# Performance work log

Measured on AMD Instinct MI355X. Metric: run time of the kernel, lower is better.

The kernel has to match this reference:

```python
import jax, jax.numpy as jnp
import numpy as np

SCALE = 256.0  # emulates SharedFxpShift = 8 fixed-point shift


def requant(x):
    # RequantFxpToScaledInt8: shift down by SharedFxpShift and clamp to int8 range
    return jnp.clip(x / SCALE, -128.0, 127.0)


def prelu(x, a):
    return jnp.where(x >= 0, x, a * x)


def _linearize(c):
    # injective encoding of 3D int coords (coords in [-8, 2040) after +8 shift)
    c = c.astype(jnp.int64) + 8
    B = 2048
    return (c[:, 0] * B + c[:, 1]) * B + c[:, 2]


def sparse_conv(coords, feats, W, stride):
    # 3x3x3 submanifold sparse conv: for each kernel offset, hash-lookup the
    # neighbor via sorted linearized coords + searchsorted, gather, matmul.
    # coords [N,3] int32, feats [N,Cin], W [27,Cin,Cout]
    lin = _linearize(coords)
    perm = jnp.argsort(lin)
    slin = lin[perm]
    N = coords.shape[0]
    out = jnp.zeros((N, W.shape[-1]), feats.dtype)
    k = 0
    for dx in (-1, 0, 1):
        for dy in (-1, 0, 1):
            for dz in (-1, 0, 1):
                off = jnp.array([dx, dy, dz], jnp.int32) * stride
                q = _linearize(coords + off[None, :])
                pos = jnp.clip(jnp.searchsorted(slin, q), 0, N - 1)
                hit = slin[pos] == q
                nb = perm[pos]
                f = jnp.where(hit[:, None], feats[nb], 0.0)
                out = out + f @ W[k]
                k += 1
    return out


def setup_inputs() -> dict:
    N, M, C = 200000, 400000, 64
    rng = np.random.default_rng(0)
    # unique parent coords: multiples of 2 in 512^3 grid
    lin = rng.choice(2 ** 24, size=N, replace=False).astype(np.int64)
    px = (lin // (256 * 256)) % 256
    py = (lin // 256) % 256
    pz = lin % 256
    rec_C = (np.stack([px, py, pz], 1) * 2).astype(np.int32)  # [N,3], stride 2
    # exactly M occupied children out of N*8, sorted (row-major mask order)
    child_idx = np.sort(rng.choice(N * 8, size=M, replace=False)).astype(np.int32)
    parent = child_idx // 8
    bit = child_idx % 8
    off = np.stack([(bit >> 2) & 1, (bit >> 1) & 1, bit & 1], 1).astype(np.int32)
    child_C = rec_C[parent] + off  # [M,3], stride 1, unique
    bins1_bits = np.zeros((N, 8), np.int32)
    bins1_bits[parent, bit] = 1
    bins0_bits = rng.integers(0, 2, size=(M, 8)).astype(np.int32)

    key = jax.random.key(0)
    ks = jax.random.split(key, 20)

    def w(k, shape, fan_in):
        return jax.random.normal(k, shape, jnp.float32) / np.sqrt(fan_in)

    inp = {
        "rec_F": jax.random.normal(ks[0], (N, C), jnp.float32) * SCALE,
        "dec_W": w(ks[1], (C + 8, C), C + 8),
        "dec_b": w(ks[2], (C,), 1) * 0.1,
        "dec_a": jnp.full((C,), 0.25, jnp.float32),
        "res_W1": w(ks[3], (27, C, C), 27 * C),
        "res_b1": w(ks[4], (C,), 1) * 0.1,
        "res_a1": jnp.full((C,), 0.25, jnp.float32),
        "res_W2": w(ks[5], (27, C, C), 27 * C),
        "res_b2": w(ks[6], (C,), 1) * 0.1,
        "p0_Wc": w(ks[7], (27, C, C), 27 * C),
        "p0_bc": w(ks[8], (C,), 1) * 0.1,
        "p0_ac": jnp.full((C,), 0.25, jnp.float32),
        "p0_Wl": w(ks[9], (C, C * 8), C),
        "p1_Wc": w(ks[10], (27, C, C), 27 * C),
        "p1_bc": w(ks[11], (C,), 1) * 0.1,
        "p1_ac": jnp.full((C,), 0.25, jnp.float32),
        "p1_Wl": w(ks[12], (C, 255), C),
        "rec_C": jnp.asarray(rec_C),
        "bins1_bits": jnp.asarray(bins1_bits),
        "child_idx": jnp.asarray(child_idx),
        "child_C": jnp.asarray(child_C),
        "bins0_bits": jnp.asarray(bins0_bits),
    }
    return inp


def reference(rec_F, dec_W, dec_b, dec_a, res_W1, res_b1, res_a1, res_W2, res_b2,
              p0_Wc, p0_bc, p0_ac, p0_Wl, p1_Wc, p1_bc, p1_ac, p1_Wl,
              rec_C, bins1_bits, child_idx, child_C, bins0_bits):
    C = dec_W.shape[1]
    # embed (empty Sequential for pred_steps=2): bins1.F << SharedFxpShift
    embed_f = bins1_bits.astype(jnp.float32) * SCALE  # [N,8]
    x = jnp.concatenate([rec_F, embed_f], 1)  # [N, C+8]
    # dec: Requant -> LinearPReLU(C+8 -> C, out32) -> ResBlock(C)
    h = requant(x)
    h = prelu(h @ dec_W + dec_b, dec_a)  # [N,C]
    r = requant(h)
    r = prelu(sparse_conv(rec_C, r, res_W1, 2) + res_b1, res_a1)
    r = requant(r)
    r = sparse_conv(rec_C, r, res_W2, 2) + res_b2
    rec_out = h + r  # [N,C]
    # pred[0]: Requant -> SparseConvPReLU(out8) -> Linear(C -> 8C, out32)
    p = requant(rec_out)
    p = requant(prelu(sparse_conv(rec_C, p, p0_Wc, 2) + p0_bc, p0_ac))
    p = p @ p0_Wl  # [N, 8C]
    # boolean-mask gather of occupied children: reshape [N,8,C] then mask ->
    # equals flat row gather with precomputed sorted child indices
    p = p.reshape(-1, C)[child_idx]  # [M,C]
    # pred[1] (last): Requant -> SparseConvPReLU(out8) -> Linear(C -> 255, out32)
    p = requant(p)
    p = requant(prelu(sparse_conv(child_C, p, p1_Wc, 1) + p1_bc, p1_ac))
    pred_out = p @ p1_Wl  # [M,255]
    # cur_oct = (cur_bins[0].F << bin2oct_kernel).sum(1) - 1
    k = jnp.arange(8, dtype=jnp.int32)
    cur_oct = ((bins0_bits << k).sum(1) - 1).astype(jnp.int16)  # [M]
    return rec_out, pred_out, cur_oct
```

## Files before the change

### kernel.cpp

```cpp
#include <hip/hip_runtime.h>
#include <stdint.h>


typedef short bf16x8 __attribute__((ext_vector_type(8)));
typedef float f32x4 __attribute__((ext_vector_type(4)));

#define EMPTY_KEY 0xFFFFFFFFu

__device__ __forceinline__ float rq(float x) {
  x *= (1.0f / 256.0f);
  return fminf(fmaxf(x, -128.0f), 127.0f);
}

__device__ __forceinline__ short f2b(float f) {
  union { float f; uint32_t u; } v; v.f = f;
  uint32_t u = v.u;
  uint32_t r = (u + 0x7FFFu + ((u >> 16) & 1u)) >> 16;
  return (short)r;
}

__device__ __forceinline__ uint32_t hkey(int x, int y, int z) {
  return ((uint32_t)(x + 8) << 20) | ((uint32_t)(y + 8) << 10) | (uint32_t)(z + 8);
}
__device__ __forceinline__ uint32_t hfun(uint32_t key, uint32_t mask) {
  return (key * 2654435761u) & mask;
}


__device__ __forceinline__ void pack_conv_elem(const float* __restrict__ W,
                                               short* __restrict__ dst, int gid) {
  int lane = gid & 63;
  int c = (gid >> 6) & 3;
  int t = (gid >> 8) & 1;
  int k = gid >> 9;
  int n = c * 16 + (lane & 15);
  int g = lane >> 4;
  bf16x8 v;
#pragma unroll
  for (int e = 0; e < 8; e++) {
    int kk = t * 32 + g * 8 + e;
    v[e] = f2b(W[(k * 64 + kk) * 64 + n]);
  }
  *(bf16x8*)(dst + gid * 8) = v;
}

__device__ __forceinline__ void pack_dense_elem(const float* __restrict__ W,
                                                short* __restrict__ dst, int K,
                                                int Ncols, int KT, int CT, int gid) {
  if (gid >= KT * CT * 64) return;
  int lane = gid & 63;
  int c = (gid >> 6) % CT;
  int t = gid / (64 * CT);
  int n = c * 16 + (lane & 15);
  int g = lane >> 4;
  bf16x8 v;
#pragma unroll
  for (int e = 0; e < 8; e++) {
    int kk = t * 32 + g * 8 + e;
    float val = (kk < K && n < Ncols) ? W[kk * Ncols + n] : 0.0f;
    v[e] = f2b(val);
  }
  *(bf16x8*)(dst + gid * 8) = v;
}

struct SetupA {
  const float *dec_W, *p0_Wl, *p1_Wl, *res_W1, *res_W2, *p0_Wc, *p1_Wc;
  const int *bins1, *child_idx, *bins0;
  uint32_t* rkeys;
  short *wpack, *decwp, *p0wp, *p1wp;
  int *bitsPk, *pStart, *bcnt;
  float* outOct;
  int N, M;
};

__global__ void __launch_bounds__(256) k_setupA(SetupA s) {
  int bid = blockIdx.x, tid = threadIdx.x;
  if (bid < 2048) {
    s.rkeys[bid * 256 + tid] = EMPTY_KEY;
    return;
  }
  bid -= 2048;
  if (bid < 216) {
    int which = bid / 54, sb = bid % 54;
    int gid = sb * 256 + tid;
    if (gid < 27 * 2 * 4 * 64) {
      const float* W = which == 0 ? s.res_W1 : which == 1 ? s.res_W2
                     : which == 2 ? s.p0_Wc : s.p1_Wc;
      pack_conv_elem(W, s.wpack + which * 110592, gid);
    }
    return;
  }
  bid -= 216;
  if (bid < 27) {
    if (bid < 3) pack_dense_elem(s.dec_W, s.decwp, 72, 64, 3, 4, bid * 256 + tid);
    else if (bid < 19) pack_dense_elem(s.p0_Wl, s.p0wp, 64, 512, 2, 32, (bid - 3) * 256 + tid);
    else pack_dense_elem(s.p1_Wl, s.p1wp, 64, 255, 2, 16, (bid - 19) * 256 + tid);
    return;
  }
  bid -= 27;
  int nbN = (s.N + 255) / 256, nbM = (s.M + 255) / 256;
  if (bid < nbN) {
    int p = bid * 256 + tid;
    if (p < s.N) {
      int b = 0;
#pragma unroll
      for (int e = 0; e < 8; e++) b |= (s.bins1[(size_t)p * 8 + e] & 1) << e;
      s.bitsPk[p] = b;
    }
    return;
  }
  bid -= nbN;
  if (bid < nbM) {
    int m = bid * 256 + tid;
    if (m < s.M) {
      int p = s.child_idx[m] >> 3;
      if (m == 0 || (s.child_idx[m - 1] >> 3) != p) s.pStart[p] = m;
    }
    return;
  }
  bid -= nbM;
  if (bid < nbM) {
    int m = bid * 256 + tid;
    if (m < s.M) {
      int ss = 0;
#pragma unroll
      for (int e = 0; e < 8; e++) ss += s.bins0[(size_t)m * 8 + e] << e;
      s.outOct[m] = (float)(ss - 1);
    }
    return;
  }
  if (tid < 8) s.bcnt[tid] = 0;
}

__global__ void __launch_bounds__(256)
k_setupB(const int* __restrict__ rec_C, const int* __restrict__ child_idx,
         uint32_t* __restrict__ rkeys, int* __restrict__ rvals,
         int* __restrict__ lists, int* __restrict__ cnt, int N, int M) {
  int bid = blockIdx.x, tid = threadIdx.x;
  int nbN = (N + 255) / 256;
  if (bid < nbN) {
    int i = bid * 256 + tid;
    if (i >= N) return;
    uint32_t key = hkey(rec_C[i * 3], rec_C[i * 3 + 1], rec_C[i * 3 + 2]);
    uint32_t s = hfun(key, (1u << 19) - 1);
    while (true) {
      uint32_t old = atomicCAS(&rkeys[s], EMPTY_KEY, key);
      if (old == EMPTY_KEY) { rvals[s] = i; return; }
      s = (s + 1) & ((1u << 19) - 1);
    }
  }
  bid -= nbN;
  __shared__ int lcnt[8];
  __shared__ int lbase[8];
  if (tid < 8) lcnt[tid] = 0;
  __syncthreads();
  int m = bid * 256 + tid;
  int b = 0, lp = 0;
  if (m < M) {
    b = child_idx[m] & 7;
    lp = atomicAdd(&lcnt[b], 1);
  }
  __syncthreads();
  if (tid < 8) lbase[tid] = atomicAdd(&cnt[tid], lcnt[tid]);
  __syncthreads();
  if (m < M) lists[(size_t)b * M + lbase[b] + lp] = m;
}

__global__ void __launch_bounds__(256)
k_setupC(const int* __restrict__ rec_C, const int* __restrict__ child_C,
         const int* __restrict__ child_idx,
         const uint32_t* __restrict__ rkeys, const int* __restrict__ rvals,
         const int* __restrict__ bitsPacked, const int* __restrict__ parentStart,
         int* __restrict__ nbrR, int* __restrict__ nbrC, int N, int M) {
  const uint32_t rmask = (1u << 19) - 1;
  int bid = blockIdx.x, tid = threadIdx.x;
  int nbRec = (N * 27 + 255) / 256;
  if (bid < nbRec) {
    int t = bid * 256 + tid;
    if (t >= N * 27) return;
    int i = t / 27, k = t % 27;
    int dx = k / 9 - 1, dy = (k / 3) % 3 - 1, dz = k % 3 - 1;
    int x = rec_C[i * 3] + dx * 2;
    int y = rec_C[i * 3 + 1] + dy * 2;
    int z = rec_C[i * 3 + 2] + dz * 2;
    uint32_t key = hkey(x, y, z);
    uint32_t s = hfun(key, rmask);
    int res = -1;
    while (true) {
      uint32_t kk = rkeys[s];
      if (kk == key) { res = rvals[s]; break; }
      if (kk == EMPTY_KEY) break;
      s = (s + 1) & rmask;
    }
    nbrR[(size_t)i * 28 + k] = res;
    return;
  }
  bid -= nbRec;
  int t = bid * 256 + tid;
  if (t >= M * 27) return;
  int m = t / 27, k = t % 27;
  int dx = k / 9 - 1, dy = (k / 3) % 3 - 1, dz = k % 3 - 1;
  int cx = child_C[(size_t)m * 3], cy = child_C[(size_t)m * 3 + 1],
      cz = child_C[(size_t)m * 3 + 2];
  int tx = cx + dx, ty = cy + dy, tz = cz + dz;
  int qx = tx >> 1, qy = ty >> 1, qz = tz >> 1;
  int r;
  if (qx == (cx >> 1) && qy == (cy >> 1) && qz == (cz >> 1)) {
    r = child_idx[m] >> 3;
  } else {
    uint32_t key = hkey(qx * 2, qy * 2, qz * 2);
    uint32_t s = hfun(key, rmask);
    r = -1;
    while (true) {
      uint32_t kk = rkeys[s];
      if (kk == key) { r = rvals[s]; break; }
      if (kk == EMPTY_KEY) break;
      s = (s + 1) & rmask;
    }
  }
  int res = -1;
  if (r >= 0) {
    int bits = bitsPacked[r];
    int bit = ((tx & 1) << 2) | ((ty & 1) << 1) | (tz & 1);
    if ((bits >> bit) & 1)
      res = parentStart[r] + __popc(bits & ((1 << bit) - 1));
  }
  nbrC[(size_t)m * 28 + k] = res;
}


__global__ void __launch_bounds__(256)
k_dec(const float* __restrict__ recF, const int* __restrict__ bits,
      const short* __restrict__ wp, const float* __restrict__ bias,
      const float* __restrict__ alpha, float* __restrict__ h32,
      short* __restrict__ hq) {
  int tid = threadIdx.x, wid = tid >> 6, lane = tid & 63;
  int rowbase = blockIdx.x * 64 + wid * 16;
  int lrow = rowbase + (lane & 15);
  int g = lane >> 4;
  f32x4 acc[4] = {};
#pragma unroll
  for (int t = 0; t < 3; t++) {
    bf16x8 a = {0, 0, 0, 0, 0, 0, 0, 0};
    if (t < 2) {
      const float* src = recF + (size_t)lrow * 64 + t * 32 + g * 8;
#pragma unroll
      for (int e = 0; e < 8; e++) a[e] = f2b(rq(src[e]));
    } else if (g == 0) {
      const int* bp = bits + (size_t)lrow * 8;
#pragma unroll
      for (int e = 0; e < 8; e++) a[e] = f2b((float)bp[e]);
    }
#pragma unroll
    for (int c = 0; c < 4; c++) {
      bf16x8 b = *(const bf16x8*)(wp + ((t * 4 + c) * 64 + lane) * 8);
      acc[c] = __builtin_amdgcn_mfma_f32_16x16x32_bf16(a, b, acc[c], 0, 0, 0);
    }
  }
#pragma unroll
  for (int c = 0; c < 4; c++) {
    int col = c * 16 + (lane & 15);
    float bi = bias[col], al = alpha[col];
#pragma unroll
    for (int r = 0; r < 4; r++) {
      int row = rowbase + g * 4 + r;
      float v = acc[c][r] + bi;
      v = v >= 0.0f ? v : al * v;
      h32[(size_t)row * 64 + col] = v;
      hq[(size_t)row * 64 + col] = f2b(rq(v));
    }
  }
}

template <int MODE>
__global__ void __launch_bounds__(256)
k_conv(const short* __restrict__ fin, const int* __restrict__ nbr,
       const short* __restrict__ wp, const float* __restrict__ bias,
       const float* __restrict__ alpha, const float* __restrict__ resid,
       float* __restrict__ out32, short* __restrict__ outq) {
  int tid = threadIdx.x, wid = tid >> 6, lane = tid & 63;
  int rowbase = blockIdx.x * 64 + wid * 16;
  int lrow = rowbase + (lane & 15);
  int g = lane >> 4;

  int4 nv[7];
#pragma unroll
  for (int j = 0; j < 7; j++)
    nv[j] = *(const int4*)(nbr + (size_t)lrow * 28 + j * 4);
  int nbk[28];
#pragma unroll
  for (int j = 0; j < 7; j++) {
    nbk[j * 4 + 0] = nv[j].x;
    nbk[j * 4 + 1] = nv[j].y;
    nbk[j * 4 + 2] = nv[j].z;
    nbk[j * 4 + 3] = nv[j].w;
  }

  f32x4 acc[4] = {};
#pragma unroll
  for (int k = 0; k < 27; k++) {
    if (__any(nbk[k] >= 0)) {
      int nb = nbk[k];
      bf16x8 a0 = {0, 0, 0, 0, 0, 0, 0, 0};
      bf16x8 a1 = {0, 0, 0, 0, 0, 0, 0, 0};
      if (nb >= 0) {
        const short* fp = fin + (size_t)nb * 64 + g * 8;
        a0 = *(const bf16x8*)fp;
        a1 = *(const bf16x8*)(fp + 32);
      }
      const short* wk = wp + k * 4096;
#pragma unroll
      for (int c = 0; c < 4; c++) {
        bf16x8 b0 = *(const bf16x8*)(wk + (c * 64 + lane) * 8);
        acc[c] = __builtin_amdgcn_mfma_f32_16x16x32_bf16(a0, b0, acc[c], 0, 0, 0);
      }
#pragma unroll
      for (int c = 0; c < 4; c++) {
        bf16x8 b1 = *(const bf16x8*)(wk + ((4 + c) * 64 + lane) * 8);
        acc[c] = __builtin_amdgcn_mfma_f32_16x16x32_bf16(a1, b1, acc[c], 0, 0, 0);
      }
    }
  }
#pragma unroll
  for (int c = 0; c < 4; c++) {
    int col = c * 16 + (lane & 15);
    float bi = bias[col];
    float al = (MODE == 0) ? alpha[col] : 0.0f;
#pragma unroll
    for (int r = 0; r < 4; r++) {
      int row = rowbase + g * 4 + r;
      float v = acc[c][r] + bi;
      if (MODE == 0) {
        v = v >= 0.0f ? v : al * v;
        outq[(size_t)row * 64 + col] = f2b(rq(v));
      } else {
        v += resid[(size_t)row * 64 + col];
        out32[(size_t)row * 64 + col] = v;
        outq[(size_t)row * 64 + col] = f2b(rq(v));
      }
    }
  }
}

__global__ void __launch_bounds__(256)
k_p0(const short* __restrict__ qq, const int* __restrict__ child_idx,
     const int* __restrict__ lists, const int* __restrict__ cnt,
     const short* __restrict__ wp, short* __restrict__ tq, int M) {
  int b = blockIdx.y;
  int cb = cnt[b];
  int start = blockIdx.x * 64;
  if (start >= cb) return;
  int tid = threadIdx.x, wid = tid >> 6, lane = tid & 63, g = lane >> 4;
  int posA = start + wid * 16 + (lane & 15);
  int parent = -1;
  if (posA < cb) parent = child_idx[lists[(size_t)b * M + posA]] >> 3;
  f32x4 acc[4] = {};
#pragma unroll
  for (int t = 0; t < 2; t++) {
    bf16x8 a = {0, 0, 0, 0, 0, 0, 0, 0};
    if (parent >= 0) a = *(const bf16x8*)(qq + (size_t)parent * 64 + t * 32 + g * 8);
#pragma unroll
    for (int c = 0; c < 4; c++) {
      bf16x8 bb = *(const bf16x8*)(wp + (((size_t)t * 32 + b * 4 + c) * 64 + lane) * 8);
      acc[c] = __builtin_amdgcn_mfma_f32_16x16x32_bf16(a, bb, acc[c], 0, 0, 0);
    }
  }
#pragma unroll
  for (int r = 0; r < 4; r++) {
    int posD = start + wid * 16 + g * 4 + r;
    if (posD < cb) {
      int m = lists[(size_t)b * M + posD];
#pragma unroll
      for (int c = 0; c < 4; c++) {
        int col = c * 16 + (lane & 15);
        tq[(size_t)m * 64 + col] = f2b(rq(acc[c][r]));
      }
    }
  }
}

__global__ void __launch_bounds__(256, 4)
k_convp1(const short* __restrict__ fin, const int* __restrict__ nbr,
         const short* __restrict__ wp, const float* __restrict__ bias,
         const float* __restrict__ alpha,
         const int* __restrict__ lists, const int* __restrict__ cnt,
         const short* __restrict__ p1wp, float* __restrict__ out, int M) {
  __shared__ short lds[4][16][64];
  __shared__ int mrow[4][16];
  int tid = threadIdx.x, wid = tid >> 6, lane = tid & 63;
  int l15 = lane & 15, g = lane >> 4;

  int pos = blockIdx.x * 64 + wid * 16 + l15;
  int m = -1;
  if (pos < M) {
    int rem = pos, b = 0;
#pragma unroll
    for (int i = 0; i < 7; i++) {
      int ci = cnt[i];
      if (b == i && rem >= ci) { rem -= ci; b = i + 1; }
    }
    m = lists[(size_t)b * M + rem];
  }
  if (g == 0) mrow[wid][l15] = m;

  int4 nv[7];
#pragma unroll
  for (int j = 0; j < 7; j++) {
    if (m >= 0) nv[j] = *(const int4*)(nbr + (size_t)m * 28 + j * 4);
    else nv[j] = make_int4(-1, -1, -1, -1);
  }
  int nbk[28];
#pragma unroll
  for (int j = 0; j < 7; j++) {
    nbk[j * 4 + 0] = nv[j].x;
    nbk[j * 4 + 1] = nv[j].y;
    nbk[j * 4 + 2] = nv[j].z;
    nbk[j * 4 + 3] = nv[j].w;
  }

  f32x4 acc[4] = {};
#pragma unroll
  for (int k = 0; k < 27; k++) {
    if (__any(nbk[k] >= 0)) {
      int nb = nbk[k];
      bf16x8 a0 = {0, 0, 0, 0, 0, 0, 0, 0};
      bf16x8 a1 = {0, 0, 0, 0, 0, 0, 0, 0};
      if (nb >= 0) {
        const short* fp = fin + (size_t)nb * 64 + g * 8;
        a0 = *(const bf16x8*)fp;
        a1 = *(const bf16x8*)(fp + 32);
      }
      const short* wk = wp + k * 4096;
#pragma unroll
      for (int c = 0; c < 4; c++) {
        bf16x8 b0 = *(const bf16x8*)(wk + (c * 64 + lane) * 8);
        acc[c] = __builtin_amdgcn_mfma_f32_16x16x32_bf16(a0, b0, acc[c], 0, 0, 0);
      }
#pragma unroll
      for (int c = 0; c < 4; c++) {
        bf16x8 b1 = *(const bf16x8*)(wk + ((4 + c) * 64 + lane) * 8);
        acc[c] = __builtin_amdgcn_mfma_f32_16x16x32_bf16(a1, b1, acc[c], 0, 0, 0);
      }
    }
  }

#pragma unroll
  for (int c = 0; c < 4; c++) {
    int col = c * 16 + l15;
    float bi = bias[col], al = alpha[col];
#pragma unroll
    for (int r = 0; r < 4; r++) {
      int rowW = g * 4 + r;
      float v = acc[c][r] + bi;
      v = v >= 0.0f ? v : al * v;
      lds[wid][rowW][col ^ ((rowW & 7) << 3)] = f2b(rq(v));
    }
  }
  __syncthreads();

  bf16x8 a0 = *(const bf16x8*)&lds[wid][l15][(g * 8) ^ ((l15 & 7) << 3)];
  bf16x8 a1 = *(const bf16x8*)&lds[wid][l15][(32 + g * 8) ^ ((l15 & 7) << 3)];
#pragma unroll
  for (int grp = 0; grp < 4; grp++) {
    f32x4 a2[4] = {};
#pragma unroll
    for (int c = 0; c < 4; c++) {
      bf16x8 b0 = *(const bf16x8*)(p1wp + ((grp * 4 + c) * 64 + lane) * 8);
      a2[c] = __builtin_amdgcn_mfma_f32_16x16x32_bf16(a0, b0, a2[c], 0, 0, 0);
      bf16x8 b1 = *(const bf16x8*)(p1wp + ((16 + grp * 4 + c) * 64 + lane) * 8);
      a2[c] = __builtin_amdgcn_mfma_f32_16x16x32_bf16(a1, b1, a2[c], 0, 0, 0);
    }
#pragma unroll
    for (int r = 0; r < 4; r++) {
      int mo = mrow[wid][g * 4 + r];
      if (mo >= 0) {
#pragma unroll
        for (int c = 0; c < 4; c++) {
          int col = (grp * 4 + c) * 16 + l15;
          if (col < 255) out[(size_t)mo * 255 + col] = a2[c][r];
        }
      }
    }
  }
}


extern "C" void kernel_launch(void* const* d_in, const int* in_sizes, int n_in,
                              void* d_out, int out_size, void* d_ws, size_t ws_size,
                              hipStream_t stream) {
  const float* rec_F  = (const float*)d_in[0];
  const float* dec_W  = (const float*)d_in[1];
  const float* dec_b  = (const float*)d_in[2];
  const float* dec_a  = (const float*)d_in[3];
  const float* res_W1 = (const float*)d_in[4];
  const float* res_b1 = (const float*)d_in[5];
  const float* res_a1 = (const float*)d_in[6];
  const float* res_W2 = (const float*)d_in[7];
  const float* res_b2 = (const float*)d_in[8];
  const float* p0_Wc  = (const float*)d_in[9];
  const float* p0_bc  = (const float*)d_in[10];
  const float* p0_ac  = (const float*)d_in[11];
  const float* p0_Wl  = (const float*)d_in[12];
  const float* p1_Wc  = (const float*)d_in[13];
  const float* p1_bc  = (const float*)d_in[14];
  const float* p1_ac  = (const float*)d_in[15];
  const float* p1_Wl  = (const float*)d_in[16];
  const int* rec_C    = (const int*)d_in[17];
  const int* bins1    = (const int*)d_in[18];
  const int* child_idx= (const int*)d_in[19];
  const int* child_C  = (const int*)d_in[20];
  const int* bins0    = (const int*)d_in[21];

  const int N = in_sizes[0] / 64;
  const int M = in_sizes[19];

  char* ws = (char*)d_ws;
  size_t off = 0;
  auto alloc = [&](size_t bytes) -> char* {
    char* p = ws + off;
    off += (bytes + 255) & ~(size_t)255;
    return p;
  };
  const uint32_t HR = 1u << 19;
  uint32_t* rkeys = (uint32_t*)alloc((size_t)HR * 4);
  int*      rvals = (int*)alloc((size_t)HR * 4);
  int* nbrR = (int*)alloc((size_t)N * 28 * 4);
  int* nbrC = (int*)alloc((size_t)M * 28 * 4);
  short* wpack = (short*)alloc((size_t)4 * 110592 * 2);
  short* decwp = (short*)alloc((size_t)3 * 4 * 64 * 8 * 2);
  short* p0wp  = (short*)alloc((size_t)2 * 32 * 64 * 8 * 2);
  short* p1wp  = (short*)alloc((size_t)2 * 16 * 64 * 8 * 2);
  short* bufA = (short*)alloc((size_t)N * 64 * 2);
  short* bufB = (short*)alloc((size_t)N * 64 * 2);
  float* h32  = (float*)alloc((size_t)N * 64 * 4);
  short* tq   = (short*)alloc((size_t)M * 64 * 2);
  int* lists  = (int*)alloc((size_t)8 * M * 4);
  int* bcnt   = (int*)alloc(256);
  int* bitsPk = (int*)alloc((size_t)N * 4);
  int* pStart = (int*)alloc((size_t)N * 4);

  float* outRec  = (float*)d_out;
  float* outPred = outRec + (size_t)N * 64;
  float* outOct  = outPred + (size_t)M * 255;

  dim3 B(256);
  int nbN = (N + 255) / 256, nbM = (M + 255) / 256;

  SetupA sa = {dec_W, p0_Wl, p1_Wl, res_W1, res_W2, p0_Wc, p1_Wc,
               bins1, child_idx, bins0, rkeys, wpack, decwp, p0wp, p1wp,
               bitsPk, pStart, bcnt, outOct, N, M};
  int gridA = 2048 + 216 + 27 + nbN + nbM + nbM + 1;
  k_setupA<<<gridA, B, 0, stream>>>(sa);
  k_setupB<<<nbN + nbM, B, 0, stream>>>(rec_C, child_idx, rkeys, rvals,
                                        lists, bcnt, N, M);
  int gridC = (N * 27 + 255) / 256 + (M * 27 + 255) / 256;
  k_setupC<<<gridC, B, 0, stream>>>(rec_C, child_C, child_idx, rkeys, rvals,
                                    bitsPk, pStart, nbrR, nbrC, N, M);

  k_dec<<<N / 64, B, 0, stream>>>(rec_F, bins1, decwp, dec_b, dec_a, h32, bufA);
  k_conv<0><<<N / 64, B, 0, stream>>>(bufA, nbrR, wpack, res_b1, res_a1,
                                      nullptr, nullptr, bufB);
  k_conv<1><<<N / 64, B, 0, stream>>>(bufB, nbrR, wpack + 110592, res_b2, nullptr,
                                      h32, outRec, bufA);
  k_conv<0><<<N / 64, B, 0, stream>>>(bufA, nbrR, wpack + 221184, p0_bc, p0_ac,
                                      nullptr, nullptr, bufB);
  k_p0<<<dim3(M / 64, 8), B, 0, stream>>>(bufB, child_idx, lists, bcnt, p0wp, tq, M);
  k_convp1<<<(M + 63) / 64, B, 0, stream>>>(tq, nbrC, wpack + 331776, p1_bc, p1_ac,
                                            lists, bcnt, p1wp, outPred, M);
}
```

Measured before the change: 690.0 us.

## Derive child neighbor maps from parent neighbor table instead of hash probes

Splits the neighbor-setup kernel in two. The child-level pass now looks up its 8 candidate parent cells from the already computed parent neighbor table (the parent neighbors at stride 2) rather than probing the hash table 27 times per child, then writes each 28-entry row with vectorized int4 stores. This removes most random hash probes for the 400k children, at the cost of an extra kernel launch and a serial dependency on the parent pass. Output stores in the residual conv and the final prediction kernel are also made nontemporal to avoid polluting cache.

```diff
diff --git a/kernel.cpp b/kernel.cpp
--- a/kernel.cpp
+++ b/kernel.cpp
@@ -167,65 +167,73 @@
 }
 
 __global__ void __launch_bounds__(256)
-k_setupC(const int* __restrict__ rec_C, const int* __restrict__ child_C,
-         const int* __restrict__ child_idx,
-         const uint32_t* __restrict__ rkeys, const int* __restrict__ rvals,
-         const int* __restrict__ bitsPacked, const int* __restrict__ parentStart,
-         int* __restrict__ nbrR, int* __restrict__ nbrC, int N, int M) {
+k_setupC1(const int* __restrict__ rec_C,
+          const uint32_t* __restrict__ rkeys, const int* __restrict__ rvals,
+          int* __restrict__ nbrR, int N) {
   const uint32_t rmask = (1u << 19) - 1;
-  int bid = blockIdx.x, tid = threadIdx.x;
-  int nbRec = (N * 27 + 255) / 256;
-  if (bid < nbRec) {
-    int t = bid * 256 + tid;
-    if (t >= N * 27) return;
-    int i = t / 27, k = t % 27;
-    int dx = k / 9 - 1, dy = (k / 3) % 3 - 1, dz = k % 3 - 1;
-    int x = rec_C[i * 3] + dx * 2;
-    int y = rec_C[i * 3 + 1] + dy * 2;
-    int z = rec_C[i * 3 + 2] + dz * 2;
-    uint32_t key = hkey(x, y, z);
-    uint32_t s = hfun(key, rmask);
-    int res = -1;
-    while (true) {
-      uint32_t kk = rkeys[s];
-      if (kk == key) { res = rvals[s]; break; }
-      if (kk == EMPTY_KEY) break;
-      s = (s + 1) & rmask;
-    }
-    nbrR[(size_t)i * 28 + k] = res;
-    return;
-  }
-  bid -= nbRec;
-  int t = bid * 256 + tid;
-  if (t >= M * 27) return;
-  int m = t / 27, k = t % 27;
+  int t = blockIdx.x * 256 + threadIdx.x;
+  if (t >= N * 27) return;
+  int i = t / 27, k = t % 27;
   int dx = k / 9 - 1, dy = (k / 3) % 3 - 1, dz = k % 3 - 1;
+  int x = rec_C[i * 3] + dx * 2;
+  int y = rec_C[i * 3 + 1] + dy * 2;
+  int z = rec_C[i * 3 + 2] + dz * 2;
+  uint32_t key = hkey(x, y, z);
+  uint32_t s = hfun(key, rmask);
+  int res = -1;
+  while (true) {
+    uint32_t kk = rkeys[s];
+    if (kk == key) { res = rvals[s]; break; }
+    if (kk == EMPTY_KEY) break;
+    s = (s + 1) & rmask;
+  }
+  nbrR[(size_t)i * 28 + k] = res;
+}
+
+__global__ void __launch_bounds__(256)
+k_setupC2(const int* __restrict__ child_C, const int* __restrict__ child_idx,
+          const int* __restrict__ nbrR, const int* __restrict__ bitsPacked,
+          const int* __restrict__ parentStart, int* __restrict__ nbrC, int M) {
+  int m = blockIdx.x * 256 + threadIdx.x;
+  if (m >= M) return;
   int cx = child_C[(size_t)m * 3], cy = child_C[(size_t)m * 3 + 1],
       cz = child_C[(size_t)m * 3 + 2];
-  int tx = cx + dx, ty = cy + dy, tz = cz + dz;
-  int qx = tx >> 1, qy = ty >> 1, qz = tz >> 1;
-  int r;
-  if (qx == (cx >> 1) && qy == (cy >> 1) && qz == (cz >> 1)) {
-    r = child_idx[m] >> 3;
-  } else {
-    uint32_t key = hkey(qx * 2, qy * 2, qz * 2);
-    uint32_t s = hfun(key, rmask);
-    r = -1;
-    while (true) {
-      uint32_t kk = rkeys[s];
-      if (kk == key) { r = rvals[s]; break; }
-      if (kk == EMPTY_KEY) break;
-      s = (s + 1) & rmask;
-    }
-  }
-  int res = -1;
-  if (r >= 0) {
-    int bits = bitsPacked[r];
+  int pr = child_idx[m] >> 3;
+  const int* nrow = nbrR + (size_t)pr * 28;
+  int px = cx & 1, py = cy & 1, pz = cz & 1;
+
+  int b8[8], s8[8];
+#pragma unroll
+  for (int j = 0; j < 8; j++) {
+    int ddx = (px - 1) + ((j >> 2) & 1);
+    int ddy = (py - 1) + ((j >> 1) & 1);
+    int ddz = (pz - 1) + (j & 1);
+    int kk = (ddx + 1) * 9 + (ddy + 1) * 3 + (ddz + 1);
+    int r = nrow[kk];
+    b8[j] = (r >= 0) ? bitsPacked[r] : 0;
+    s8[j] = (r >= 0) ? parentStart[r] : 0;
+  }
+
+  int nout[28];
+  nout[27] = -1;
+#pragma unroll
+  for (int k = 0; k < 27; k++) {
+    const int dx = k / 9 - 1, dy = (k / 3) % 3 - 1, dz = k % 3 - 1;
+    int tx = cx + dx, ty = cy + dy, tz = cz + dz;
+    int jx = ((px + dx + 2) >> 1) - px;
+    int jy = ((py + dy + 2) >> 1) - py;
+    int jz = ((pz + dz + 2) >> 1) - pz;
+    int j = jx * 4 + jy * 2 + jz;
     int bit = ((tx & 1) << 2) | ((ty & 1) << 1) | (tz & 1);
-    if ((bits >> bit) & 1)
-      res = parentStart[r] + __popc(bits & ((1 << bit) - 1));
-  }
-  nbrC[(size_t)m * 28 + k] = res;
+    int bits = b8[j];
+    int res = -1;
+    if ((bits >> bit) & 1) res = s8[j] + __popc(bits & ((1 << bit) - 1));
+    nout[k] = res;
+  }
+#pragma unroll
+  for (int q = 0; q < 7; q++)
+    *(int4*)(nbrC + (size_t)m * 28 + q * 4) =
+        make_int4(nout[q * 4], nout[q * 4 + 1], nout[q * 4 + 2], nout[q * 4 + 3]);
 }
 
 
@@ -335,7 +343,7 @@
         outq[(size_t)row * 64 + col] = f2b(rq(v));
       } else {
         v += resid[(size_t)row * 64 + col];
-        out32[(size_t)row * 64 + col] = v;
+        __builtin_nontemporal_store(v, &out32[(size_t)row * 64 + col]);
         outq[(size_t)row * 64 + col] = f2b(rq(v));
       }
     }
@@ -477,7 +485,8 @@
 #pragma unroll
         for (int c = 0; c < 4; c++) {
           int col = (grp * 4 + c) * 16 + l15;
-          if (col < 255) out[(size_t)mo * 255 + col] = a2[c][r];
+          if (col < 255)
+            __builtin_nontemporal_store(a2[c][r], &out[(size_t)mo * 255 + col]);
         }
       }
     }
@@ -553,9 +562,9 @@
   k_setupA<<<gridA, B, 0, stream>>>(sa);
   k_setupB<<<nbN + nbM, B, 0, stream>>>(rec_C, child_idx, rkeys, rvals,
                                         lists, bcnt, N, M);
-  int gridC = (N * 27 + 255) / 256 + (M * 27 + 255) / 256;
-  k_setupC<<<gridC, B, 0, stream>>>(rec_C, child_C, child_idx, rkeys, rvals,
-                                    bitsPk, pStart, nbrR, nbrC, N, M);
+  k_setupC1<<<(N * 27 + 255) / 256, B, 0, stream>>>(rec_C, rkeys, rvals, nbrR, N);
+  k_setupC2<<<nbM, B, 0, stream>>>(child_C, child_idx, nbrR, bitsPk, pStart,
+                                   nbrC, M);
 
   k_dec<<<N / 64, B, 0, stream>>>(rec_F, bins1, decwp, dec_b, dec_a, h32, bufA);
   k_conv<0><<<N / 64, B, 0, stream>>>(bufA, nbrR, wpack, res_b1, res_a1,
```

Result: faster. 631.4 us (-8.5%).
